# Optimization experiments

Measured on AMD Instinct MI355X. Metric: run time of the kernel, lower is better.

Reference implementation:

```python
import jax, jax.numpy as jnp
import numpy as np

B, T, D = 2, 2048, 1024
NH, DH = 16, 64  # inner = NH*DH = D
SCALE_INIT = 0.02


def setup_inputs() -> dict:
    key = jax.random.key(0)
    kx, kq, kk, kv, ko = jax.random.split(key, 5)
    return {
        "x": jax.random.normal(kx, (B, T, D), dtype=jnp.float32),
        "Wq": jax.random.normal(kq, (D, NH * DH), dtype=jnp.float32) * SCALE_INIT,
        "Wk": jax.random.normal(kk, (D, NH * DH), dtype=jnp.float32) * SCALE_INIT,
        "Wv": jax.random.normal(kv, (D, NH * DH), dtype=jnp.float32) * SCALE_INIT,
        "Wo": jax.random.normal(ko, (NH * DH, D), dtype=jnp.float32) * SCALE_INIT,
    }


def reference(x, Wq, Wk, Wv, Wo):
    # x: (B, T, D)
    b, t, _ = x.shape

    def split_heads(h):
        # (B, T, NH*DH) -> (B, NH, T, DH)
        return h.reshape(b, t, NH, DH).transpose(0, 2, 1, 3)

    q = split_heads(x @ Wq)
    k = split_heads(x @ Wk)
    v = split_heads(x @ Wv)

    scale = jnp.asarray(1.0 / np.sqrt(DH), dtype=x.dtype)
    # The per-chunk loop in the original is mathematically equivalent to
    # full causal attention: each query row attends to keys with k_pos <= q_pos.
    scores = jnp.einsum("bhqd,bhkd->bhqk", q, k) * scale  # (B, NH, T, T)
    causal_mask = jnp.arange(t)[None, :] > jnp.arange(t)[:, None]  # k_pos > q_pos
    scores = jnp.where(causal_mask, -jnp.inf, scores)
    attn = jax.nn.softmax(scores, axis=-1)
    attn = jnp.nan_to_num(attn)  # matches torch.nan_to_num (no fully-masked rows in causal case)
    o = jnp.einsum("bhqk,bhkd->bhqd", attn, v)  # (B, NH, T, DH)
    o = o.transpose(0, 2, 1, 3).reshape(b, t, NH * DH)  # merge heads
    return o @ Wo  # (B, T, D)
```

## Files before the change

### kernel.cpp

```cpp
#include <hip/hip_runtime.h>
#include <hip/hip_bf16.h>
#include <string.h>

#define Bsz 2
#define Tsz 2048
#define Dsz 1024
#define NHsz 16
#define Msz (Bsz*Tsz)

typedef unsigned short bfu;
typedef __attribute__((ext_vector_type(8))) short short8;
typedef __attribute__((ext_vector_type(4))) short short4v;
typedef __attribute__((ext_vector_type(4))) float floatx4;

__device__ __forceinline__ bfu f2bf(float f) {
  unsigned int u = __builtin_bit_cast(unsigned int, f);
  u += 0x7fffu + ((u >> 16) & 1u);
  return (bfu)(u >> 16);
}

__device__ __forceinline__ short4v pack4bf(float a, float b, float c_, float d) {
  __hip_bfloat162 h01 = __float22bfloat162_rn(make_float2(a, b));
  __hip_bfloat162 h23 = __float22bfloat162_rn(make_float2(c_, d));
  uint2 uu;
  memcpy(&uu.x, &h01, 4);
  memcpy(&uu.y, &h23, 4);
  return __builtin_bit_cast(short4v, uu);
}

__device__ __forceinline__ short8 pack8bf(float4 a, float4 b) {
  __hip_bfloat162 h0 = __float22bfloat162_rn(make_float2(a.x, a.y));
  __hip_bfloat162 h1 = __float22bfloat162_rn(make_float2(a.z, a.w));
  __hip_bfloat162 h2 = __float22bfloat162_rn(make_float2(b.x, b.y));
  __hip_bfloat162 h3 = __float22bfloat162_rn(make_float2(b.z, b.w));
  uint4 u;
  memcpy(&u.x, &h0, 4); memcpy(&u.y, &h1, 4);
  memcpy(&u.z, &h2, 4); memcpy(&u.w, &h3, 4);
  return __builtin_bit_cast(short8, u);
}

__device__ __forceinline__ void async16(const void* g, void* l) {
  void* gnc = (void*)g;
  __builtin_amdgcn_global_load_lds((__attribute__((address_space(1))) void*)gnc,
                                   (__attribute__((address_space(3))) void*)l,
                                   16, 0, 0);
}

__global__ __launch_bounds__(256) void transpose_w(const float* __restrict__ W0, const float* __restrict__ W1,
                                                   const float* __restrict__ W2, const float* __restrict__ W3,
                                                   bfu* __restrict__ wt) {
  __shared__ float tile[32][33];
  const float* W = blockIdx.z == 0 ? W0 : blockIdx.z == 1 ? W1 : blockIdx.z == 2 ? W2 : W3;
  bfu* WT = wt + (size_t)blockIdx.z * Dsz * Dsz;
  int tx = threadIdx.x, ty = threadIdx.y;
  int kb = blockIdx.y * 32, nb = blockIdx.x * 32;
#pragma unroll
  for (int i = 0; i < 4; ++i)
    tile[ty + i*8][tx] = W[(size_t)(kb + ty + i*8) * Dsz + nb + tx];
  __syncthreads();
#pragma unroll
  for (int i = 0; i < 4; ++i)
    WT[(size_t)(nb + ty + i*8) * Dsz + kb + tx] = f2bf(tile[tx][ty + i*8]);
}

template <bool F32OUT, bool AF32>
__global__ __launch_bounds__(256) void gemm128(const void* __restrict__ Ain, const bfu* __restrict__ Bt0,
                                               void* __restrict__ C0, int K, int N,
                                               size_t strideB, size_t strideC, float scale0) {
  const int tid = threadIdx.x, wave = tid >> 6, lane = tid & 63;
  const int g = lane >> 4, c = lane & 15;
  const int m0 = blockIdx.y * 128, n0 = blockIdx.x * 128;
  const bfu* Bt = Bt0 + strideB * blockIdx.z;
  const float scale = (blockIdx.z == 0) ? scale0 : 1.0f;
  __shared__ bfu As[128 * 32];
  __shared__ bfu Bs[128 * 32];
  floatx4 acc[4][4] = {};
  const int srow = lane >> 2, scol = (lane & 3) * 8;
  const bfu* gB = Bt + (size_t)(n0 + srow) * K + scol;
  const int wm = (wave >> 1) * 64, wn = (wave & 1) * 64;

  short8 areg[2];
  if (AF32) {
#pragma unroll
    for (int cc = 0; cc < 2; ++cc) {
      const float* pa = (const float*)Ain +
          (size_t)(m0 + (wave*2 + cc)*16 + srow) * K + scol;
      areg[cc] = pack8bf(((const float4*)pa)[0], ((const float4*)pa)[1]);
    }
  }
  const bfu* gA = AF32 ? nullptr : (const bfu*)Ain + (size_t)(m0 + srow) * K + scol;

  for (int k0 = 0; k0 < K; k0 += 32) {
    __syncthreads();
#pragma unroll
    for (int cc = 0; cc < 2; ++cc) {
      const int chunk = wave * 2 + cc;
      if (AF32) *(short8*)&As[chunk * 512 + lane * 8] = areg[cc];
      else      async16(gA + (size_t)chunk * 16 * K + k0, &As[chunk * 512]);
      async16(gB + (size_t)chunk * 16 * K + k0, &Bs[chunk * 512]);
    }
    __syncthreads();
    if (AF32 && k0 + 32 < K) {
#pragma unroll
      for (int cc = 0; cc < 2; ++cc) {
        const float* pa = (const float*)Ain +
            (size_t)(m0 + (wave*2 + cc)*16 + srow) * K + (k0 + 32) + scol;
        areg[cc] = pack8bf(((const float4*)pa)[0], ((const float4*)pa)[1]);
      }
    }
    short8 afr[4], bfr[4];
#pragma unroll
    for (int t = 0; t < 4; ++t) afr[t] = *(const short8*)&As[(wm + t*16 + c) * 32 + g * 8];
#pragma unroll
    for (int t = 0; t < 4; ++t) bfr[t] = *(const short8*)&Bs[(wn + t*16 + c) * 32 + g * 8];
#pragma unroll
    for (int i = 0; i < 4; ++i)
#pragma unroll
      for (int j = 0; j < 4; ++j)
        acc[i][j] = __builtin_amdgcn_mfma_f32_16x16x32_bf16(afr[i], bfr[j], acc[i][j], 0, 0, 0);
  }
  const bool vtrans = (!F32OUT) && (blockIdx.z == 2);
#pragma unroll
  for (int i = 0; i < 4; ++i) {
#pragma unroll
    for (int j = 0; j < 4; ++j) {
      const int m = m0 + wm + i*16 + g*4;
      const int n = n0 + wn + j*16 + c;
      if (vtrans) {
        bfu* vtp = (bfu*)C0 + (size_t)2 * strideC;
        size_t o = ((size_t)((m >> 11) * 16 + (n >> 6)) * 64 + (n & 63)) * Tsz + (m & 2047);
        *(short4v*)&vtp[o] = pack4bf(acc[i][j][0], acc[i][j][1], acc[i][j][2], acc[i][j][3]);
      } else {
#pragma unroll
        for (int r = 0; r < 4; ++r) {
          float v = acc[i][j][r] * scale;
          if (F32OUT) ((float*)C0)[(size_t)(m + r) * N + n] = v;
          else        ((bfu*)C0)[strideC * blockIdx.z + (size_t)(m + r) * N + n] = f2bf(v);
        }
      }
    }
  }
}

__global__ __launch_bounds__(256, 2) void attn_kernel(const bfu* __restrict__ qkv,
                                                      bfu* __restrict__ obuf) {
  const int tid = threadIdx.x, wave = tid >> 6, lane = tid & 63;
  const int g = (lane >> 4) & 3, c = lane & 15, c7 = c & 7;
  const int bh = blockIdx.y, b = bh >> 4, h = bh & 15;
  const size_t hb = (size_t)b * Tsz * Dsz + h * 64;
  const bfu* Qp = qkv + hb;
  const bfu* Kp = qkv + (size_t)Msz * Dsz + hb;
  const bfu* Vt = qkv + (size_t)2 * Msz * Dsz + (size_t)bh * 64 * Tsz;

  __shared__ bfu Ks[128 * 64];
  __shared__ bfu Vs[64 * 128];
  __shared__ bfu Ps[4][16 * 128];

  const int krow_in = lane >> 3;
  const int kcol_g  = (((lane & 7) ^ krow_in) << 3);
  const int kcol_s  = ((lane & 7) << 3);
  const int vrow_in = lane >> 4;
  const int vcol_s  = ((lane & 15) << 3);

  for (int half = 0; half < 2; ++half) {
    const int j = half ? (31 - (int)blockIdx.x) : (int)blockIdx.x;
    const int qw = j * 64 + wave * 16;
    const int ktm = j >> 1;

    short8 bq[2];
#pragma unroll
    for (int kk = 0; kk < 2; ++kk)
      bq[kk] = *(const short8*)(Qp + (size_t)(qw + c) * Dsz + kk * 32 + g * 8);

    floatx4 acc[4] = {};
    float mi = -3.0e38f, li = 0.0f;

    short8 kreg[4], vreg[4];
#pragma unroll
    for (int cc = 0; cc < 4; ++cc) {
      const int ch = wave * 4 + cc;
      kreg[cc] = *(const short8*)(Kp + (size_t)(ch * 8 + krow_in) * Dsz + kcol_g);
      const int drow = ch * 4 + vrow_in;
      vreg[cc] = *(const short8*)(Vt + (size_t)drow * Tsz + (((lane & 15) ^ (drow & 7)) << 3));
    }

    for (int kt = 0; kt <= ktm; ++kt) {
      __syncthreads();
#pragma unroll
      for (int cc = 0; cc < 4; ++cc) {
        const int ch = wave * 4 + cc;
        *(short8*)&Ks[(ch * 8 + krow_in) * 64 + kcol_s] = kreg[cc];
        const int drow = ch * 4 + vrow_in;
        *(short8*)&Vs[drow * 128 + vcol_s] = vreg[cc];
      }
      __syncthreads();
      if (kt < ktm) {
#pragma unroll
        for (int cc = 0; cc < 4; ++cc) {
          const int ch = wave * 4 + cc;
          kreg[cc] = *(const short8*)(Kp + (size_t)((kt+1)*128 + ch*8 + krow_in) * Dsz + kcol_g);
          const int drow = ch * 4 + vrow_in;
          vreg[cc] = *(const short8*)(Vt + (size_t)drow * Tsz + (kt+1)*128 +
                                      (((lane & 15) ^ (drow & 7)) << 3));
        }
      }

      floatx4 st[8] = {};
#pragma unroll
      for (int kk = 0; kk < 2; ++kk)
#pragma unroll
        for (int mk = 0; mk < 8; ++mk) {
          const short8 kf = *(const short8*)&Ks[(mk * 16 + c) * 64 + (((kk * 4 + g) ^ c7) << 3)];
          st[mk] = __builtin_amdgcn_mfma_f32_16x16x32_bf16(kf, bq[kk], st[mk], 0, 0, 0);
        }

      if (kt == ktm) {
#pragma unroll
        for (int mk = 0; mk < 8; ++mk) {
          const int keyb = kt * 128 + mk * 16 + g * 4;
#pragma unroll
          for (int r = 0; r < 4; ++r)
            if (keyb + r > qw + c) st[mk][r] = -1.0e38f;
        }
      }

      float mloc = -3.0e38f;
#pragma unroll
      for (int mk = 0; mk < 8; ++mk)
#pragma unroll
        for (int r = 0; r < 4; ++r) mloc = fmaxf(mloc, st[mk][r]);
      mloc = fmaxf(mloc, __shfl_xor(mloc, 16));
      mloc = fmaxf(mloc, __shfl_xor(mloc, 32));
      const float mnew = fmaxf(mi, mloc);
      const float alpha = exp2f(mi - mnew);
      mi = mnew;
      float sum = 0.0f;
#pragma unroll
      for (int mk = 0; mk < 8; ++mk) {
        float pr[4];
#pragma unroll
        for (int r = 0; r < 4; ++r) { pr[r] = exp2f(st[mk][r] - mnew); sum += pr[r]; }
        *(short4v*)&Ps[wave][c * 128 + (((mk * 2 + (g >> 1)) ^ c7) << 3) + ((g & 1) << 2)] =
            pack4bf(pr[0], pr[1], pr[2], pr[3]);
      }
      sum += __shfl_xor(sum, 16);
      sum += __shfl_xor(sum, 32);
      li = li * alpha + sum;

      float al[4];
#pragma unroll
      for (int r = 0; r < 4; ++r) al[r] = __shfl(alpha, (lane & 48) | (g * 4 + r));
#pragma unroll
      for (int nd = 0; nd < 4; ++nd)
#pragma unroll
        for (int r = 0; r < 4; ++r) acc[nd][r] *= al[r];

#pragma unroll
      for (int kc = 0; kc < 4; ++kc) {
        const int sl = ((kc * 4 + g) ^ c7) << 3;
        const short8 pf = *(const short8*)&Ps[wave][c * 128 + sl];
#pragma unroll
        for (int nd = 0; nd < 4; ++nd) {
          const short8 vf = *(const short8*)&Vs[(nd * 16 + c) * 128 + sl];
          acc[nd] = __builtin_amdgcn_mfma_f32_16x16x32_bf16(pf, vf, acc[nd], 0, 0, 0);
        }
      }
    }

    float inv[4];
#pragma unroll
    for (int r = 0; r < 4; ++r) inv[r] = 1.0f / __shfl(li, (lane & 48) | (g * 4 + r));
#pragma unroll
    for (int nd = 0; nd < 4; ++nd)
#pragma unroll
      for (int r = 0; r < 4; ++r)
        obuf[(size_t)(b * Tsz + qw + g * 4 + r) * Dsz + h * 64 + nd * 16 + c] =
            f2bf(acc[nd][r] * inv[r]);
  }
}

extern "C" void kernel_launch(void* const* d_in, const int* in_sizes, int n_in,
                              void* d_out, int out_size, void* d_ws, size_t ws_size,
                              hipStream_t stream) {
  const float* x  = (const float*)d_in[0];
  const float* Wq = (const float*)d_in[1];
  const float* Wk = (const float*)d_in[2];
  const float* Wv = (const float*)d_in[3];
  const float* Wo = (const float*)d_in[4];
  float* out = (float*)d_out;

  bfu* wt   = (bfu*)d_ws;
  bfu* qkv  = wt  + (size_t)4 * Dsz * Dsz;
  bfu* obuf = qkv + (size_t)3 * Msz * Dsz;

  transpose_w<<<dim3(32, 32, 4), dim3(32, 8), 0, stream>>>(Wq, Wk, Wv, Wo, wt);
  gemm128<false, true><<<dim3(Dsz / 128, Msz / 128, 3), dim3(256), 0, stream>>>(
      (const void*)x, wt, (void*)qkv, Dsz, Dsz, (size_t)Dsz * Dsz, (size_t)Msz * Dsz,
      0.125f * 1.44269504088896f);
  attn_kernel<<<dim3(16, Bsz * NHsz), dim3(256), 0, stream>>>(qkv, obuf);
  gemm128<true, false><<<dim3(Dsz / 128, Msz / 128, 1), dim3(256), 0, stream>>>(
      (const void*)obuf, wt + (size_t)3 * Dsz * Dsz, (void*)out, Dsz, Dsz,
      (size_t)0, (size_t)0, 1.0f);
}
```

Baseline: 210.9 us.

## Stage V-transpose via LDS, narrow output GEMM tiles, async K/V loads in attention

The QKV GEMM now writes the transposed V through a swizzled shared-memory staging buffer, so global stores become coalesced 16-byte rows instead of scattered 8-byte writes. The output projection GEMM gets a template N-tile width and runs with 64-wide tiles, doubling its block count to fill more CUs. In attention, the register-prefetched K/V tiles are replaced by direct async global-to-LDS copies each iteration. That removes register staging and the overlap of the next tile's loads with compute, which may expose load latency.

```diff
diff --git a/kernel.cpp b/kernel.cpp
--- a/kernel.cpp
+++ b/kernel.cpp
@@ -63,21 +63,23 @@
     WT[(size_t)(nb + ty + i*8) * Dsz + kb + tx] = f2bf(tile[tx][ty + i*8]);
 }
 
-template <bool F32OUT, bool AF32>
+template <bool F32OUT, bool AF32, int NT>
 __global__ __launch_bounds__(256) void gemm128(const void* __restrict__ Ain, const bfu* __restrict__ Bt0,
                                                void* __restrict__ C0, int K, int N,
                                                size_t strideB, size_t strideC, float scale0) {
+  constexpr int NJ = NT / 32;
   const int tid = threadIdx.x, wave = tid >> 6, lane = tid & 63;
   const int g = lane >> 4, c = lane & 15;
-  const int m0 = blockIdx.y * 128, n0 = blockIdx.x * 128;
+  const int m0 = blockIdx.y * 128, n0 = blockIdx.x * NT;
   const bfu* Bt = Bt0 + strideB * blockIdx.z;
   const float scale = (blockIdx.z == 0) ? scale0 : 1.0f;
-  __shared__ bfu As[128 * 32];
-  __shared__ bfu Bs[128 * 32];
-  floatx4 acc[4][4] = {};
+  __shared__ bfu smem[4096 + NT * 32];
+  bfu* As = smem;
+  bfu* Bs = smem + 4096;
+  floatx4 acc[4][NJ] = {};
   const int srow = lane >> 2, scol = (lane & 3) * 8;
   const bfu* gB = Bt + (size_t)(n0 + srow) * K + scol;
-  const int wm = (wave >> 1) * 64, wn = (wave & 1) * 64;
+  const int wm = (wave >> 1) * 64, wn = (wave & 1) * (NT / 2);
 
   short8 areg[2];
   if (AF32) {
@@ -97,6 +99,10 @@
       const int chunk = wave * 2 + cc;
       if (AF32) *(short8*)&As[chunk * 512 + lane * 8] = areg[cc];
       else      async16(gA + (size_t)chunk * 16 * K + k0, &As[chunk * 512]);
+    }
+#pragma unroll
+    for (int cc = 0; cc < NT/64; ++cc) {
+      const int chunk = wave * (NT/64) + cc;
       async16(gB + (size_t)chunk * 16 * K + k0, &Bs[chunk * 512]);
     }
     __syncthreads();
@@ -108,35 +114,61 @@
         areg[cc] = pack8bf(((const float4*)pa)[0], ((const float4*)pa)[1]);
       }
     }
-    short8 afr[4], bfr[4];
+    short8 afr[4], bfr[NJ];
 #pragma unroll
     for (int t = 0; t < 4; ++t) afr[t] = *(const short8*)&As[(wm + t*16 + c) * 32 + g * 8];
 #pragma unroll
-    for (int t = 0; t < 4; ++t) bfr[t] = *(const short8*)&Bs[(wn + t*16 + c) * 32 + g * 8];
+    for (int t = 0; t < NJ; ++t) bfr[t] = *(const short8*)&Bs[(wn + t*16 + c) * 32 + g * 8];
 #pragma unroll
     for (int i = 0; i < 4; ++i)
 #pragma unroll
-      for (int j = 0; j < 4; ++j)
+      for (int j = 0; j < NJ; ++j)
         acc[i][j] = __builtin_amdgcn_mfma_f32_16x16x32_bf16(afr[i], bfr[j], acc[i][j], 0, 0, 0);
   }
-  const bool vtrans = (!F32OUT) && (blockIdx.z == 2);
+
+  const bool vtrans = (!F32OUT) && (NT == 128) && (blockIdx.z == 2);
+  if (vtrans) {
+    bfu* vtp = (bfu*)C0 + (size_t)2 * strideC;
+#pragma unroll
+    for (int p = 0; p < 2; ++p) {
+      __syncthreads();
+      if ((wave & 1) == p) {
+#pragma unroll
+        for (int i = 0; i < 4; ++i)
+#pragma unroll
+          for (int j = 0; j < NJ; ++j) {
+            const int nl = j*16 + c;
+            const int mg = ((wm + i*16) >> 3) + (g >> 1);
+            const int phys = nl * 128 + ((mg ^ (nl & 15)) << 3) + ((g & 1) << 2);
+            *(short4v*)&smem[phys] = pack4bf(acc[i][j][0], acc[i][j][1],
+                                             acc[i][j][2], acc[i][j][3]);
+          }
+      }
+      __syncthreads();
+      const int h_ = (n0 + p * 64) >> 6;
+      bfu* dst = vtp + ((size_t)((m0 >> 11) * 16 + h_) * 64) * Tsz + (m0 & 2047);
+#pragma unroll
+      for (int s = 0; s < 4; ++s) {
+        const int nl = s * 16 + (tid >> 4);
+        const int me = (tid & 15) << 3;
+        const int phys = nl * 128 + (((me >> 3) ^ (nl & 15)) << 3);
+        *(short8*)&dst[(size_t)nl * Tsz + me] = *(const short8*)&smem[phys];
+      }
+    }
+    return;
+  }
+
 #pragma unroll
   for (int i = 0; i < 4; ++i) {
 #pragma unroll
-    for (int j = 0; j < 4; ++j) {
+    for (int j = 0; j < NJ; ++j) {
       const int m = m0 + wm + i*16 + g*4;
       const int n = n0 + wn + j*16 + c;
-      if (vtrans) {
-        bfu* vtp = (bfu*)C0 + (size_t)2 * strideC;
-        size_t o = ((size_t)((m >> 11) * 16 + (n >> 6)) * 64 + (n & 63)) * Tsz + (m & 2047);
-        *(short4v*)&vtp[o] = pack4bf(acc[i][j][0], acc[i][j][1], acc[i][j][2], acc[i][j][3]);
-      } else {
-#pragma unroll
-        for (int r = 0; r < 4; ++r) {
-          float v = acc[i][j][r] * scale;
-          if (F32OUT) ((float*)C0)[(size_t)(m + r) * N + n] = v;
-          else        ((bfu*)C0)[strideC * blockIdx.z + (size_t)(m + r) * N + n] = f2bf(v);
-        }
+#pragma unroll
+      for (int r = 0; r < 4; ++r) {
+        float v = acc[i][j][r] * scale;
+        if (F32OUT) ((float*)C0)[(size_t)(m + r) * N + n] = v;
+        else        ((bfu*)C0)[strideC * blockIdx.z + (size_t)(m + r) * N + n] = f2bf(v);
       }
     }
   }
@@ -156,11 +188,9 @@
   __shared__ bfu Vs[64 * 128];
   __shared__ bfu Ps[4][16 * 128];
 
-  const int krow_in = lane >> 3;
-  const int kcol_g  = (((lane & 7) ^ krow_in) << 3);
-  const int kcol_s  = ((lane & 7) << 3);
-  const int vrow_in = lane >> 4;
-  const int vcol_s  = ((lane & 15) << 3);
+  const int kst_row = lane >> 3;
+  const int kst_off = ((lane & 7) ^ kst_row) << 3;
+  const int vst_row = lane >> 4;
 
   for (int half = 0; half < 2; ++half) {
     const int j = half ? (31 - (int)blockIdx.x) : (int)blockIdx.x;
@@ -175,35 +205,16 @@
     floatx4 acc[4] = {};
     float mi = -3.0e38f, li = 0.0f;
 
-    short8 kreg[4], vreg[4];
-#pragma unroll
-    for (int cc = 0; cc < 4; ++cc) {
-      const int ch = wave * 4 + cc;
-      kreg[cc] = *(const short8*)(Kp + (size_t)(ch * 8 + krow_in) * Dsz + kcol_g);
-      const int drow = ch * 4 + vrow_in;
-      vreg[cc] = *(const short8*)(Vt + (size_t)drow * Tsz + (((lane & 15) ^ (drow & 7)) << 3));
-    }
-
     for (int kt = 0; kt <= ktm; ++kt) {
       __syncthreads();
 #pragma unroll
       for (int cc = 0; cc < 4; ++cc) {
         const int ch = wave * 4 + cc;
-        *(short8*)&Ks[(ch * 8 + krow_in) * 64 + kcol_s] = kreg[cc];
-        const int drow = ch * 4 + vrow_in;
-        *(short8*)&Vs[drow * 128 + vcol_s] = vreg[cc];
+        async16(Kp + (size_t)(kt * 128 + ch * 8 + kst_row) * Dsz + kst_off, &Ks[ch * 512]);
+        const int drow = ch * 4 + vst_row;
+        async16(Vt + (size_t)drow * Tsz + kt * 128 + (((lane & 15) ^ (drow & 7)) << 3), &Vs[ch * 512]);
       }
       __syncthreads();
-      if (kt < ktm) {
-#pragma unroll
-        for (int cc = 0; cc < 4; ++cc) {
-          const int ch = wave * 4 + cc;
-          kreg[cc] = *(const short8*)(Kp + (size_t)((kt+1)*128 + ch*8 + krow_in) * Dsz + kcol_g);
-          const int drow = ch * 4 + vrow_in;
-          vreg[cc] = *(const short8*)(Vt + (size_t)drow * Tsz + (kt+1)*128 +
-                                      (((lane & 15) ^ (drow & 7)) << 3));
-        }
-      }
 
       floatx4 st[8] = {};
 #pragma unroll
@@ -294,11 +305,11 @@
   bfu* obuf = qkv + (size_t)3 * Msz * Dsz;
 
   transpose_w<<<dim3(32, 32, 4), dim3(32, 8), 0, stream>>>(Wq, Wk, Wv, Wo, wt);
-  gemm128<false, true><<<dim3(Dsz / 128, Msz / 128, 3), dim3(256), 0, stream>>>(
+  gemm128<false, true, 128><<<dim3(Dsz / 128, Msz / 128, 3), dim3(256), 0, stream>>>(
       (const void*)x, wt, (void*)qkv, Dsz, Dsz, (size_t)Dsz * Dsz, (size_t)Msz * Dsz,
       0.125f * 1.44269504088896f);
   attn_kernel<<<dim3(16, Bsz * NHsz), dim3(256), 0, stream>>>(qkv, obuf);
-  gemm128<true, false><<<dim3(Dsz / 128, Msz / 128, 1), dim3(256), 0, stream>>>(
+  gemm128<true, false, 64><<<dim3(Dsz / 64, Msz / 128, 1), dim3(256), 0, stream>>>(
       (const void*)obuf, wt + (size_t)3 * Dsz * Dsz, (void*)out, Dsz, Dsz,
       (size_t)0, (size_t)0, 1.0f);
 }
```

Result: faster. 202.6 us (-3.9%).
